# Kernel tuning notes

Measured on AMD Instinct MI355X. Metric: run time of the kernel, lower is better.

Reference implementation:

```python
import jax, jax.numpy as jnp
import numpy as np

IN_FEATURES = 4096
OUT_FEATURES = 11008
GROUPSIZE = 128
N_GROUPS = IN_FEATURES // GROUPSIZE  # 32


def setup_inputs() -> dict:
    key = jax.random.key(0)
    k1, k2, k3 = jax.random.split(key, 3)
    inp = jax.random.normal(k1, (2, 2048, IN_FEATURES), dtype=jnp.float32)
    # int8 quantized weights stored as int8
    weight = jax.random.randint(k2, (OUT_FEATURES, IN_FEATURES), -128, 128, dtype=jnp.int32).astype(jnp.int8)
    # per-(output-channel, group) positive scales
    scales = jax.random.uniform(k3, (OUT_FEATURES, N_GROUPS), dtype=jnp.float32) * 0.01 + 1e-4
    return {"input": inp, "weight": weight, "scales": scales}


def reference(input, weight, scales):
    # Dequantize: w[o, g, j] = int8_w[o, g, j] * scales[o, g]
    O, I = weight.shape
    w = weight.astype(input.dtype).reshape(O, N_GROUPS, GROUPSIZE)
    w = (w * scales[:, :, None].astype(input.dtype)).reshape(O, I)
    # F.linear: input @ w.T  -> [B, S, O]
    return jnp.einsum("bsi,oi->bso", input, w)
```

## Files before the change

### kernel.cpp

```cpp
#include <hip/hip_runtime.h>

#define MDIM 4096
#define KDIM 4096
#define NDIM 11008
#define NGROUPS 32

#define BM 256
#define BN 256
#define BK 64
#define NT (KDIM / BK)
#define KB (KDIM * 2)

typedef _Float16 f16x8 __attribute__((ext_vector_type(8)));
typedef float f32x4 __attribute__((ext_vector_type(4)));

typedef const unsigned int __attribute__((address_space(1))) *gas_t;
typedef unsigned int __attribute__((address_space(3))) *las_t;

__device__ __forceinline__ void gld_lds16(const void *g, void *l) {
  __builtin_amdgcn_global_load_lds((gas_t)g, (las_t)l, 16, 0, 0);
}

#define BAR() asm volatile("s_barrier" ::: "memory")
#define VMW4() asm volatile("s_waitcnt vmcnt(4)" ::: "memory")
#define VMW0() asm volatile("s_waitcnt vmcnt(0)" ::: "memory")
#define FENCE() __builtin_amdgcn_sched_barrier(0)

__global__ __launch_bounds__(256) void cvt_a_kernel(const float *__restrict__ a,
                                                    _Float16 *__restrict__ o) {
  const int n8 = (MDIM * KDIM) / 8;
  for (int i = blockIdx.x * blockDim.x + threadIdx.x; i < n8;
       i += gridDim.x * blockDim.x) {
    const float4 v0 = *(const float4 *)(a + (size_t)i * 8);
    const float4 v1 = *(const float4 *)(a + (size_t)i * 8 + 4);
    f16x8 h;
    h[0] = (_Float16)v0.x; h[1] = (_Float16)v0.y;
    h[2] = (_Float16)v0.z; h[3] = (_Float16)v0.w;
    h[4] = (_Float16)v1.x; h[5] = (_Float16)v1.y;
    h[6] = (_Float16)v1.z; h[7] = (_Float16)v1.w;
    *(f16x8 *)(o + (size_t)i * 8) = h;
  }
}

__global__ __launch_bounds__(256) void cvt_w_kernel(const int *__restrict__ w,
                                                    const float *__restrict__ s,
                                                    _Float16 *__restrict__ o) {
  const int n8 = (NDIM * KDIM) / 8;
  for (int i = blockIdx.x * blockDim.x + threadIdx.x; i < n8;
       i += gridDim.x * blockDim.x) {
    const size_t base = (size_t)i * 8;
    const int row = (int)(base >> 12);
    const int g = ((int)(base & (KDIM - 1))) >> 7;
    const float sc = s[row * NGROUPS + g];
    const int4 w0 = *(const int4 *)(w + base);
    const int4 w1 = *(const int4 *)(w + base + 4);
    f16x8 h;
    h[0] = (_Float16)((float)w0.x * sc); h[1] = (_Float16)((float)w0.y * sc);
    h[2] = (_Float16)((float)w0.z * sc); h[3] = (_Float16)((float)w0.w * sc);
    h[4] = (_Float16)((float)w1.x * sc); h[5] = (_Float16)((float)w1.y * sc);
    h[6] = (_Float16)((float)w1.z * sc); h[7] = (_Float16)((float)w1.w * sc);
    *(f16x8 *)(o + base) = h;
  }
}

__global__ __launch_bounds__(512, 2) void gemm_8phase(
    const _Float16 *__restrict__ Ah, const _Float16 *__restrict__ Wh,
    float *__restrict__ C) {
  __shared__ __align__(16) _Float16 As[2][BM * BK];
  __shared__ __align__(16) _Float16 Bs[2][BN * BK];

  const int tid = threadIdx.x;
  const int l = tid & 63;
  const int w = tid >> 6;
  const int wm = w >> 2;
  const int wn = w & 3;

  const int wg = blockIdx.x;
  const int swz = (wg & 7) * 86 + (wg >> 3);
  const int bx = swz / 16;
  const int by = swz % 16;

  const int srow = l >> 3;
  const int gk = ((l & 7) ^ srow) * 16;
  const char *Ag =
      (const char *)Ah + (size_t)(by * BM + w * 8 + srow) * KB + gk;
  const char *Bg =
      (const char *)Wh + (size_t)(bx * BN + w * 8 + srow) * KB + gk;

  const int laneRow = (l & 15) * (BK * 2);
  const int kx0 = ((l >> 4) * 16) ^ ((l & 7) * 16);
  const int kx1 = kx0 ^ 64;

  f32x4 acc[8][4] = {};
  f16x8 af0[4][2], af1[4][2], bf0[2][2], bf1[2][2];

#define STAGE2_A(KT, B, S0)                                                   \
  {                                                                           \
    const char *ap_ = Ag + (size_t)(KT) * (BK * 2);                           \
    gld_lds16(ap_ + (size_t)(S0) * (64 * KB),                                 \
              (void *)&As[B][(S0) * 4096 + w * 512]);                         \
    gld_lds16(ap_ + (size_t)((S0) + 1) * (64 * KB),                           \
              (void *)&As[B][((S0) + 1) * 4096 + w * 512]);                   \
  }

#define STAGE2_B(KT, B, S0)                                                   \
  {                                                                           \
    const char *bp_ = Bg + (size_t)(KT) * (BK * 2);                           \
    gld_lds16(bp_ + (size_t)(S0) * (64 * KB),                                 \
              (void *)&Bs[B][(S0) * 4096 + w * 512]);                         \
    gld_lds16(bp_ + (size_t)((S0) + 1) * (64 * KB),                           \
              (void *)&Bs[B][((S0) + 1) * 4096 + w * 512]);                   \
  }

#define LDA_Q(DST, QM, BASE)                                                  \
  {                                                                           \
    const char *ba_ = (BASE) + (wm * 128 + (QM) * 64) * (BK * 2) + laneRow;   \
    _Pragma("unroll") for (int mi = 0; mi < 4; ++mi) {                        \
      DST[mi][0] = *(const f16x8 *)(ba_ + mi * 2048 + kx0);                   \
      DST[mi][1] = *(const f16x8 *)(ba_ + mi * 2048 + kx1);                   \
    }                                                                         \
  }

#define LDB_Q(DST, QN, BASE)                                                  \
  {                                                                           \
    const char *bb_ = (BASE) + (wn * 64 + (QN) * 32) * (BK * 2) + laneRow;    \
    _Pragma("unroll") for (int nj = 0; nj < 2; ++nj) {                        \
      DST[nj][0] = *(const f16x8 *)(bb_ + nj * 2048 + kx0);                   \
      DST[nj][1] = *(const f16x8 *)(bb_ + nj * 2048 + kx1);                   \
    }                                                                         \
  }

#define MMA_Q(AF, BF, QM, QN)                                                 \
  __builtin_amdgcn_s_setprio(1);                                              \
  _Pragma("unroll") for (int ks = 0; ks < 2; ++ks)                            \
      _Pragma("unroll") for (int mi = 0; mi < 4; ++mi)                        \
          _Pragma("unroll") for (int nj = 0; nj < 2; ++nj)                    \
              acc[(QM) * 4 + mi][(QN) * 2 + nj] =                             \
                  __builtin_amdgcn_mfma_f32_16x16x32_f16(                     \
                      AF[mi][ks], BF[nj][ks],                                 \
                      acc[(QM) * 4 + mi][(QN) * 2 + nj], 0, 0, 0);            \
  __builtin_amdgcn_s_setprio(0);

  STAGE2_A(0, 0, 0); STAGE2_A(0, 0, 2);
  STAGE2_B(0, 0, 0); STAGE2_B(0, 0, 2);
  STAGE2_B(1, 1, 0); STAGE2_B(1, 1, 2);
  VMW4();
  BAR();
  LDA_Q(af0, 0, (const char *)&As[0][0]);
  LDB_Q(bf0, 0, (const char *)&Bs[0][0]);

#pragma unroll 2
  for (int t = 0; t < NT; ++t) {
    const int b = t & 1;
    const char *Ab = (const char *)&As[b][0];
    const char *Bb = (const char *)&Bs[b][0];
    const char *An = (const char *)&As[b ^ 1][0];
    const char *Bn = (const char *)&Bs[b ^ 1][0];
    const bool s1 = (t + 1 < NT);
    const bool s2 = (t + 2 < NT);

    LDB_Q(bf1, 1, Bb);
    if (s1) STAGE2_A(t + 1, b ^ 1, 0);
    FENCE();
    MMA_Q(af0, bf0, 0, 0);

    LDA_Q(af1, 1, Ab);
    if (s1) STAGE2_A(t + 1, b ^ 1, 2);
    FENCE();
    MMA_Q(af0, bf1, 0, 1);
    BAR();

    if (s2) STAGE2_B(t + 2, b, 0);
    FENCE();
    MMA_Q(af1, bf1, 1, 1);

    if (s2) STAGE2_B(t + 2, b, 2);
    FENCE();
    MMA_Q(af1, bf0, 1, 0);
    if (s2) { VMW4(); } else { VMW0(); }
    BAR();
    if (s1) {
      LDA_Q(af0, 0, An);
      LDB_Q(bf0, 0, Bn);
    }
  }

#undef STAGE2_A
#undef STAGE2_B
#undef LDA_Q
#undef LDB_Q
#undef MMA_Q

  const int fr = l & 15, fq = l >> 4;
  float *Cb = C + (size_t)(by * BM + wm * 128) * NDIM + bx * BN + wn * 64;
#pragma unroll
  for (int i = 0; i < 8; ++i)
#pragma unroll
    for (int j = 0; j < 4; ++j)
#pragma unroll
      for (int r = 0; r < 4; ++r)
        Cb[(size_t)(i * 16 + fq * 4 + r) * NDIM + j * 16 + fr] = acc[i][j][r];
}

__global__ __launch_bounds__(256) void gemm_fused(const float *__restrict__ A,
                                                  const int *__restrict__ W,
                                                  const float *__restrict__ S,
                                                  float *__restrict__ C) {
  __shared__ _Float16 Asf[128 * 64];
  __shared__ _Float16 Bsf[128 * 64];
  const int tid = threadIdx.x;
  const int lane = tid & 63;
  const int wv = tid >> 6;
  const int wm = wv >> 1, wn = wv & 1;
  const int bx = blockIdx.x, by = blockIdx.y;
  const int srow = tid >> 1;
  const int skof = (tid & 1) * 32;

  const float *Ab = A + (size_t)(by * 128 + srow) * KDIM + skof;
  const int *Wb = W + (size_t)(bx * 128 + srow) * KDIM + skof;
  const float *Sb = S + (size_t)(bx * 128 + srow) * NGROUPS;

  f32x4 acc[4][4] = {};
  float4 ar[8];
  int4 wr[8];
  float sc;

#pragma unroll
  for (int u = 0; u < 8; ++u) {
    ar[u] = *(const float4 *)(Ab + u * 4);
    wr[u] = *(const int4 *)(Wb + u * 4);
  }
  sc = Sb[0];

  const int fr = lane & 15;
  const int fq = lane >> 4;
  const int kbase = fq * 8;

  for (int kt = 0; kt < KDIM / 64; ++kt) {
    __syncthreads();
    _Float16 *Ad = &Asf[srow * 64 + skof];
    _Float16 *Bd = &Bsf[srow * 64 + skof];
#pragma unroll
    for (int u = 0; u < 4; ++u) {
      const float4 a0 = ar[2 * u], a1 = ar[2 * u + 1];
      const int4 b0 = wr[2 * u], b1 = wr[2 * u + 1];
      f16x8 ha, hb;
      ha[0] = (_Float16)a0.x; ha[1] = (_Float16)a0.y;
      ha[2] = (_Float16)a0.z; ha[3] = (_Float16)a0.w;
      ha[4] = (_Float16)a1.x; ha[5] = (_Float16)a1.y;
      ha[6] = (_Float16)a1.z; ha[7] = (_Float16)a1.w;
      hb[0] = (_Float16)((float)b0.x * sc); hb[1] = (_Float16)((float)b0.y * sc);
      hb[2] = (_Float16)((float)b0.z * sc); hb[3] = (_Float16)((float)b0.w * sc);
      hb[4] = (_Float16)((float)b1.x * sc); hb[5] = (_Float16)((float)b1.y * sc);
      hb[6] = (_Float16)((float)b1.z * sc); hb[7] = (_Float16)((float)b1.w * sc);
      *(f16x8 *)(Ad + u * 8) = ha;
      *(f16x8 *)(Bd + u * 8) = hb;
    }
    if (kt + 1 < KDIM / 64) {
      const float *An = Ab + (kt + 1) * 64;
      const int *Wn = Wb + (kt + 1) * 64;
#pragma unroll
      for (int u = 0; u < 8; ++u) {
        ar[u] = *(const float4 *)(An + u * 4);
        wr[u] = *(const int4 *)(Wn + u * 4);
      }
      sc = Sb[(kt + 1) >> 1];
    }
    __syncthreads();
#pragma unroll
    for (int ks = 0; ks < 2; ++ks) {
      f16x8 afv[4], bfv[4];
      const int kof = ks * 32 + kbase;
#pragma unroll
      for (int i = 0; i < 4; ++i) {
        afv[i] = *(const f16x8 *)&Asf[(wm * 64 + i * 16 + fr) * 64 + kof];
        bfv[i] = *(const f16x8 *)&Bsf[(wn * 64 + i * 16 + fr) * 64 + kof];
      }
#pragma unroll
      for (int i = 0; i < 4; ++i)
#pragma unroll
        for (int j = 0; j < 4; ++j)
          acc[i][j] = __builtin_amdgcn_mfma_f32_16x16x32_f16(afv[i], bfv[j],
                                                             acc[i][j], 0, 0, 0);
    }
  }

  float *Cb = C + (size_t)(by * 128 + wm * 64) * NDIM + bx * 128 + wn * 64;
#pragma unroll
  for (int i = 0; i < 4; ++i)
#pragma unroll
    for (int j = 0; j < 4; ++j)
#pragma unroll
      for (int r = 0; r < 4; ++r)
        Cb[(size_t)(i * 16 + fq * 4 + r) * NDIM + j * 16 + fr] = acc[i][j][r];
}

extern "C" void kernel_launch(void *const *d_in, const int *in_sizes, int n_in,
                              void *d_out, int out_size, void *d_ws,
                              size_t ws_size, hipStream_t stream) {
  (void)in_sizes; (void)n_in; (void)out_size;
  const float *A = (const float *)d_in[0];
  const int *W = (const int *)d_in[1];
  const float *S = (const float *)d_in[2];
  float *C = (float *)d_out;

  const size_t needA = (size_t)MDIM * KDIM * sizeof(_Float16);
  const size_t needW = (size_t)NDIM * KDIM * sizeof(_Float16);

  if (ws_size >= needA + needW) {
    _Float16 *Ahp = (_Float16 *)d_ws;
    _Float16 *Whp = (_Float16 *)((char *)d_ws + needA);
    cvt_a_kernel<<<2048, 256, 0, stream>>>(A, Ahp);
    cvt_w_kernel<<<2048, 256, 0, stream>>>(W, S, Whp);
    gemm_8phase<<<(MDIM / BM) * (NDIM / BN), 512, 0, stream>>>(Ahp, Whp, C);
  } else {
    dim3 grid(NDIM / 128, MDIM / 128);
    gemm_fused<<<grid, 256, 0, stream>>>(A, W, S, C);
  }
}
```

Measured before the change: 475.1 us.

## Prefetch A two tiles ahead and overlap next-tile fragment loads with last MMA

```diff
diff --git a/kernel.cpp b/kernel.cpp
--- a/kernel.cpp
+++ b/kernel.cpp
@@ -22,7 +22,7 @@
 }
 
 #define BAR() asm volatile("s_barrier" ::: "memory")
-#define VMW4() asm volatile("s_waitcnt vmcnt(4)" ::: "memory")
+#define VMW8() asm volatile("s_waitcnt vmcnt(8)" ::: "memory")
 #define VMW0() asm volatile("s_waitcnt vmcnt(0)" ::: "memory")
 #define FENCE() __builtin_amdgcn_sched_barrier(0)
 
@@ -141,50 +141,54 @@
                       acc[(QM) * 4 + mi][(QN) * 2 + nj], 0, 0, 0);            \
   __builtin_amdgcn_s_setprio(0);
 
+#define TILE_BODY(TT, BIDX, B0r, B1r)                                         \
+  {                                                                           \
+    const char *Ab = (const char *)&As[BIDX][0];                              \
+    const char *Bb = (const char *)&Bs[BIDX][0];                              \
+    const char *An = (const char *)&As[(BIDX) ^ 1][0];                        \
+    const char *Bn = (const char *)&Bs[(BIDX) ^ 1][0];                        \
+    const bool s1 = ((TT) + 1 < NT);                                          \
+    const bool s2 = ((TT) + 2 < NT);                                          \
+          \
+    LDB_Q(B1r, 1, Bb);                                                        \
+    FENCE();                                                                  \
+    MMA_Q(af0, B0r, 0, 0);                                                    \
+                   \
+    LDA_Q(af1, 1, Ab);                                                        \
+    FENCE();                                                                  \
+    MMA_Q(af0, B1r, 0, 1);                                                    \
+    BAR();          \
+                            \
+    if (s2) { STAGE2_B((TT) + 2, BIDX, 0); STAGE2_B((TT) + 2, BIDX, 2); }     \
+    FENCE();                                                                  \
+    MMA_Q(af1, B1r, 1, 1);                                                    \
+    BAR();          \
+         \
+          \
+    if (s2) { STAGE2_A((TT) + 2, BIDX, 0); STAGE2_A((TT) + 2, BIDX, 2);       \
+              VMW8(); }                                                       \
+    else { VMW0(); }                                                          \
+    BAR();                             \
+    if (s1) { LDA_Q(af0, 0, An); LDB_Q(B1r, 0, Bn); }                         \
+    FENCE();                                                                  \
+    MMA_Q(af1, B0r, 1, 0);                                                    \
+  }
+
   STAGE2_A(0, 0, 0); STAGE2_A(0, 0, 2);
   STAGE2_B(0, 0, 0); STAGE2_B(0, 0, 2);
+  STAGE2_A(1, 1, 0); STAGE2_A(1, 1, 2);
   STAGE2_B(1, 1, 0); STAGE2_B(1, 1, 2);
-  VMW4();
+  VMW8();
   BAR();
   LDA_Q(af0, 0, (const char *)&As[0][0]);
   LDB_Q(bf0, 0, (const char *)&Bs[0][0]);
 
-#pragma unroll 2
-  for (int t = 0; t < NT; ++t) {
-    const int b = t & 1;
-    const char *Ab = (const char *)&As[b][0];
-    const char *Bb = (const char *)&Bs[b][0];
-    const char *An = (const char *)&As[b ^ 1][0];
-    const char *Bn = (const char *)&Bs[b ^ 1][0];
-    const bool s1 = (t + 1 < NT);
-    const bool s2 = (t + 2 < NT);
-
-    LDB_Q(bf1, 1, Bb);
-    if (s1) STAGE2_A(t + 1, b ^ 1, 0);
-    FENCE();
-    MMA_Q(af0, bf0, 0, 0);
-
-    LDA_Q(af1, 1, Ab);
-    if (s1) STAGE2_A(t + 1, b ^ 1, 2);
-    FENCE();
-    MMA_Q(af0, bf1, 0, 1);
-    BAR();
-
-    if (s2) STAGE2_B(t + 2, b, 0);
-    FENCE();
-    MMA_Q(af1, bf1, 1, 1);
-
-    if (s2) STAGE2_B(t + 2, b, 2);
-    FENCE();
-    MMA_Q(af1, bf0, 1, 0);
-    if (s2) { VMW4(); } else { VMW0(); }
-    BAR();
-    if (s1) {
-      LDA_Q(af0, 0, An);
-      LDB_Q(bf0, 0, Bn);
-    }
-  }
-
+  for (int t = 0; t < NT; t += 2) {
+    TILE_BODY(t, 0, bf0, bf1);
+    TILE_BODY(t + 1, 1, bf1, bf0);
+  }
+
+#undef TILE_BODY
 #undef STAGE2_A
 #undef STAGE2_B
 #undef LDA_Q
```

Measured after the change: 506.8 us. 6.7% more time.

## Switch main GEMM from 16x16x32 to 32x32x16 MFMA tiles

Applied to the files above, without the earlier changes.

```diff
diff --git a/kernel.cpp b/kernel.cpp
--- a/kernel.cpp
+++ b/kernel.cpp
@@ -13,6 +13,7 @@
 
 typedef _Float16 f16x8 __attribute__((ext_vector_type(8)));
 typedef float f32x4 __attribute__((ext_vector_type(4)));
+typedef float f32x16 __attribute__((ext_vector_type(16)));
 
 typedef const unsigned int __attribute__((address_space(1))) *gas_t;
 typedef unsigned int __attribute__((address_space(3))) *las_t;
@@ -87,12 +88,15 @@
   const char *Bg =
       (const char *)Wh + (size_t)(bx * BN + w * 8 + srow) * KB + gk;
 
-  const int laneRow = (l & 15) * (BK * 2);
-  const int kx0 = ((l >> 4) * 16) ^ ((l & 7) * 16);
-  const int kx1 = kx0 ^ 64;
-
-  f32x4 acc[8][4] = {};
-  f16x8 af0[4][2], af1[4][2], bf0[2][2], bf1[2][2];
+  const int laneRow32 = (l & 31) * 128;
+  int kxs[4];
+#pragma unroll
+  for (int kk = 0; kk < 4; ++kk)
+    kxs[kk] = ((((kk << 1) | (l >> 5)) ^ (l & 7)) << 4);
+
+  f32x16 acc[4][2] = {};
+  f16x8 af0[2][4], af1[2][4];
+  f16x8 bf0[4], bf1[4];
 
 #define STAGE2_A(KT, B, S0)                                                   \
   {                                                                           \
@@ -114,31 +118,25 @@
 
 #define LDA_Q(DST, QM, BASE)                                                  \
   {                                                                           \
-    const char *ba_ = (BASE) + (wm * 128 + (QM) * 64) * (BK * 2) + laneRow;   \
-    _Pragma("unroll") for (int mi = 0; mi < 4; ++mi) {                        \
-      DST[mi][0] = *(const f16x8 *)(ba_ + mi * 2048 + kx0);                   \
-      DST[mi][1] = *(const f16x8 *)(ba_ + mi * 2048 + kx1);                   \
-    }                                                                         \
+    const char *ba_ = (BASE) + (wm * 128 + (QM) * 64) * (BK * 2) + laneRow32; \
+    _Pragma("unroll") for (int mi = 0; mi < 2; ++mi)                          \
+        _Pragma("unroll") for (int kk = 0; kk < 4; ++kk)                      \
+            DST[mi][kk] = *(const f16x8 *)(ba_ + mi * 4096 + kxs[kk]);        \
   }
 
 #define LDB_Q(DST, QN, BASE)                                                  \
   {                                                                           \
-    const char *bb_ = (BASE) + (wn * 64 + (QN) * 32) * (BK * 2) + laneRow;    \
-    _Pragma("unroll") for (int nj = 0; nj < 2; ++nj) {                        \
-      DST[nj][0] = *(const f16x8 *)(bb_ + nj * 2048 + kx0);                   \
-      DST[nj][1] = *(const f16x8 *)(bb_ + nj * 2048 + kx1);                   \
-    }                                                                         \
+    const char *bb_ = (BASE) + (wn * 64 + (QN) * 32) * (BK * 2) + laneRow32;  \
+    _Pragma("unroll") for (int kk = 0; kk < 4; ++kk)                          \
+        DST[kk] = *(const f16x8 *)(bb_ + kxs[kk]);                            \
   }
 
 #define MMA_Q(AF, BF, QM, QN)                                                 \
   __builtin_amdgcn_s_setprio(1);                                              \
-  _Pragma("unroll") for (int ks = 0; ks < 2; ++ks)                            \
-      _Pragma("unroll") for (int mi = 0; mi < 4; ++mi)                        \
-          _Pragma("unroll") for (int nj = 0; nj < 2; ++nj)                    \
-              acc[(QM) * 4 + mi][(QN) * 2 + nj] =                             \
-                  __builtin_amdgcn_mfma_f32_16x16x32_f16(                     \
-                      AF[mi][ks], BF[nj][ks],                                 \
-                      acc[(QM) * 4 + mi][(QN) * 2 + nj], 0, 0, 0);            \
+  _Pragma("unroll") for (int kk = 0; kk < 4; ++kk)                            \
+      _Pragma("unroll") for (int mi = 0; mi < 2; ++mi)                        \
+          acc[(QM) * 2 + mi][QN] = __builtin_amdgcn_mfma_f32_32x32x16_f16(    \
+              AF[mi][kk], BF[kk], acc[(QM) * 2 + mi][QN], 0, 0, 0);           \
   __builtin_amdgcn_s_setprio(0);
 
   STAGE2_A(0, 0, 0); STAGE2_A(0, 0, 2);
@@ -191,15 +189,18 @@
 #undef LDB_Q
 #undef MMA_Q
 
-  const int fr = l & 15, fq = l >> 4;
-  float *Cb = C + (size_t)(by * BM + wm * 128) * NDIM + bx * BN + wn * 64;
-#pragma unroll
-  for (int i = 0; i < 8; ++i)
-#pragma unroll
-    for (int j = 0; j < 4; ++j)
-#pragma unroll
-      for (int r = 0; r < 4; ++r)
-        Cb[(size_t)(i * 16 + fq * 4 + r) * NDIM + j * 16 + fr] = acc[i][j][r];
+  const int col = l & 31;
+  const int hh = l >> 5;
+  float *Cb = C + (size_t)(by * BM + wm * 128) * NDIM + bx * BN + wn * 64 + col;
+#pragma unroll
+  for (int ai = 0; ai < 4; ++ai)
+#pragma unroll
+    for (int nj = 0; nj < 2; ++nj)
+#pragma unroll
+      for (int r = 0; r < 16; ++r) {
+        const int row = ai * 32 + (r & 3) + 8 * (r >> 2) + 4 * hh;
+        Cb[(size_t)row * NDIM + nj * 32] = acc[ai][nj][r];
+      }
 }
 
 __global__ __launch_bounds__(256) void gemm_fused(const float *__restrict__ A,
```

Result: no change. 481.3 us (+1.3%).

## Triple-buffer B tiles in LDS and drop the mid-iteration barrier

Applied to the files above, without the earlier changes.

```diff
diff --git a/kernel.cpp b/kernel.cpp
--- a/kernel.cpp
+++ b/kernel.cpp
@@ -66,8 +66,7 @@
 __global__ __launch_bounds__(512, 2) void gemm_8phase(
     const _Float16 *__restrict__ Ah, const _Float16 *__restrict__ Wh,
     float *__restrict__ C) {
-  __shared__ __align__(16) _Float16 As[2][BM * BK];
-  __shared__ __align__(16) _Float16 Bs[2][BN * BK];
+  __shared__ __align__(16) char Sh[163840];
 
   const int tid = threadIdx.x;
   const int l = tid & 63;
@@ -94,22 +93,25 @@
   f32x4 acc[8][4] = {};
   f16x8 af0[4][2], af1[4][2], bf0[2][2], bf1[2][2];
 
-#define STAGE2_A(KT, B, S0)                                                   \
+  unsigned aC = 0, aN = 32768;
+  unsigned bC = 65536, bN = 98304, bS = 131072;
+
+#define STAGE2_A(KT, OFF, S0)                                                 \
   {                                                                           \
     const char *ap_ = Ag + (size_t)(KT) * (BK * 2);                           \
     gld_lds16(ap_ + (size_t)(S0) * (64 * KB),                                 \
-              (void *)&As[B][(S0) * 4096 + w * 512]);                         \
+              (void *)(Sh + (OFF) + (S0) * 8192 + w * 1024));                 \
     gld_lds16(ap_ + (size_t)((S0) + 1) * (64 * KB),                           \
-              (void *)&As[B][((S0) + 1) * 4096 + w * 512]);                   \
-  }
-
-#define STAGE2_B(KT, B, S0)                                                   \
+              (void *)(Sh + (OFF) + ((S0) + 1) * 8192 + w * 1024));           \
+  }
+
+#define STAGE2_B(KT, OFF, S0)                                                 \
   {                                                                           \
     const char *bp_ = Bg + (size_t)(KT) * (BK * 2);                           \
     gld_lds16(bp_ + (size_t)(S0) * (64 * KB),                                 \
-              (void *)&Bs[B][(S0) * 4096 + w * 512]);                         \
+              (void *)(Sh + (OFF) + (S0) * 8192 + w * 1024));                 \
     gld_lds16(bp_ + (size_t)((S0) + 1) * (64 * KB),                           \
-              (void *)&Bs[B][((S0) + 1) * 4096 + w * 512]);                   \
+              (void *)(Sh + (OFF) + ((S0) + 1) * 8192 + w * 1024));           \
   }
 
 #define LDA_Q(DST, QM, BASE)                                                  \
@@ -141,48 +143,46 @@
                       acc[(QM) * 4 + mi][(QN) * 2 + nj], 0, 0, 0);            \
   __builtin_amdgcn_s_setprio(0);
 
-  STAGE2_A(0, 0, 0); STAGE2_A(0, 0, 2);
-  STAGE2_B(0, 0, 0); STAGE2_B(0, 0, 2);
-  STAGE2_B(1, 1, 0); STAGE2_B(1, 1, 2);
+  STAGE2_A(0, aC, 0); STAGE2_A(0, aC, 2);
+  STAGE2_B(0, bC, 0); STAGE2_B(0, bC, 2);
+  STAGE2_B(1, bN, 0); STAGE2_B(1, bN, 2);
   VMW4();
   BAR();
-  LDA_Q(af0, 0, (const char *)&As[0][0]);
-  LDB_Q(bf0, 0, (const char *)&Bs[0][0]);
+  LDA_Q(af0, 0, (const char *)Sh + aC);
+  LDB_Q(bf0, 0, (const char *)Sh + bC);
 
 #pragma unroll 2
   for (int t = 0; t < NT; ++t) {
-    const int b = t & 1;
-    const char *Ab = (const char *)&As[b][0];
-    const char *Bb = (const char *)&Bs[b][0];
-    const char *An = (const char *)&As[b ^ 1][0];
-    const char *Bn = (const char *)&Bs[b ^ 1][0];
     const bool s1 = (t + 1 < NT);
     const bool s2 = (t + 2 < NT);
-
-    LDB_Q(bf1, 1, Bb);
-    if (s1) STAGE2_A(t + 1, b ^ 1, 0);
+    const char *Ac = (const char *)Sh + aC;
+    const char *An = (const char *)Sh + aN;
+    const char *Bc = (const char *)Sh + bC;
+    const char *Bn = (const char *)Sh + bN;
+
+    if (s1) { STAGE2_A(t + 1, aN, 0); STAGE2_A(t + 1, aN, 2); }
+    if (s2) { STAGE2_B(t + 2, bS, 0); STAGE2_B(t + 2, bS, 2); }
+
+    LDB_Q(bf1, 1, Bc);
     FENCE();
     MMA_Q(af0, bf0, 0, 0);
 
-    LDA_Q(af1, 1, Ab);
-    if (s1) STAGE2_A(t + 1, b ^ 1, 2);
+    LDA_Q(af1, 1, Ac);
     FENCE();
     MMA_Q(af0, bf1, 0, 1);
-    BAR();
-
-    if (s2) STAGE2_B(t + 2, b, 0);
-    FENCE();
+
     MMA_Q(af1, bf1, 1, 1);
-
-    if (s2) STAGE2_B(t + 2, b, 2);
-    FENCE();
     MMA_Q(af1, bf0, 1, 0);
+
     if (s2) { VMW4(); } else { VMW0(); }
     BAR();
     if (s1) {
       LDA_Q(af0, 0, An);
       LDB_Q(bf0, 0, Bn);
     }
+
+    { const unsigned ta = aC; aC = aN; aN = ta; }
+    { const unsigned tb = bC; bC = bN; bN = bS; bS = tb; }
   }
 
 #undef STAGE2_A
```

Result: faster. 409.1 us (-13.9%).
